# Optimization experiments

Measured on AMD Instinct MI355X. Metric: run time of the kernel, lower is better.

Reference implementation:

```python
import jax, jax.numpy as jnp
import numpy as np
from jax import lax

EPS = 1e-6


def _layernorm(x, g, b, eps=1e-5):
    m = x.mean(-1, keepdims=True)
    v = x.var(-1, keepdims=True)
    return (x - m) / jnp.sqrt(v + eps) * g + b


def _causal_conv(x, w, b, dilation):
    # x: [B,S,D], w: [K, D_in, D_out] -> causal (left) padded dilated conv + GELU, residual
    k = w.shape[0]
    pad = (k - 1) * dilation
    y = lax.conv_general_dilated(
        x, w, window_strides=(1,), padding=[(pad, 0)], rhs_dilation=(dilation,),
        dimension_numbers=('NWC', 'WIO', 'NWC'))
    return x + jax.nn.gelu(y + b)


def setup_inputs() -> dict:
    key = jax.random.key(0)
    B, S, D, DC, N_LTM, K_WM, KS = 4, 2048, 1024, 256, 768, 8, 5
    ks = jax.random.split(key, 24)
    sc = 0.02

    def n(k, shape, scale=sc):
        return jax.random.normal(k, shape, jnp.float32) * scale

    return {
        'x': jax.random.normal(ks[0], (B, S, D), jnp.float32),
        'cache': jax.random.normal(ks[1], (B, N_LTM, DC), jnp.float32),
        'wm': jax.random.normal(ks[2], (B, K_WM, DC + 1), jnp.float32),
        # LTM read projections
        'Wq_ltm': n(ks[3], (D, DC)), 'Wo_ltm': n(ks[4], (DC, D)), 'wg_ltm': n(ks[5], (D,)),
        # WM read projections
        'Wq_wm': n(ks[6], (D, DC)), 'Wo_wm': n(ks[7], (DC, D)), 'wg_wm': n(ks[8], (D,)),
        # causal dilated conv stack (2 layers, k=5, dilations 1 and 2)
        'conv1_w': n(ks[9], (KS, D, D)), 'conv1_b': jnp.zeros((D,), jnp.float32),
        'conv2_w': n(ks[10], (KS, D, D)), 'conv2_b': jnp.zeros((D,), jnp.float32),
        'ln_g': jnp.ones((D,), jnp.float32), 'ln_b': jnp.zeros((D,), jnp.float32),
        # WM write (learned slot keys for addressing)
        'Wqw_wm': n(ks[11], (D, DC)), 'Ww_wm': n(ks[12], (D, DC)),
        'wm_keys': n(ks[13], (K_WM, DC), 1.0), 'wgw_wm': n(ks[14], (D,)),
        # LTM write (content-based addressing against cache)
        'Wqw_ltm': n(ks[15], (D, DC)), 'Ww_ltm': n(ks[16], (D, DC)), 'wgw_ltm': n(ks[17], (D,)),
    }


def reference(x, cache, wm, Wq_ltm, Wo_ltm, wg_ltm, Wq_wm, Wo_wm, wg_wm,
              conv1_w, conv1_b, conv2_w, conv2_b, ln_g, ln_b,
              Wqw_wm, Ww_wm, wm_keys, wgw_wm, Wqw_ltm, Ww_ltm, wgw_ltm):
    DC = cache.shape[-1]
    inv_sqrt = 1.0 / jnp.sqrt(jnp.float32(DC))

    # ---- LTM READ: content-addressed soft read, gated residual blend ----
    q = x @ Wq_ltm                                                  # [B,S,DC]
    attn = jax.nn.softmax(jnp.einsum('bsd,bnd->bsn', q, cache) * inv_sqrt, -1)
    read = jnp.einsum('bsn,bnd->bsd', attn, cache)                  # [B,S,DC]
    gate = jax.nn.sigmoid(x @ wg_ltm)[..., None]                    # [B,S,1]
    x_ltm = x + gate * (read @ Wo_ltm)

    # ---- WM READ (read_decay=0.0 -> wm unchanged by read) ----
    content = wm[..., :DC]                                          # [B,Kw,DC]
    q2 = x_ltm @ Wq_wm
    attn2 = jax.nn.softmax(jnp.einsum('bsd,bkd->bsk', q2, content) * inv_sqrt, -1)
    read2 = jnp.einsum('bsk,bkd->bsd', attn2, content)
    gate2 = jax.nn.sigmoid(x_ltm @ wg_wm)[..., None]
    x_enh = x_ltm + gate2 * (read2 @ Wo_wm)

    # ---- COMPUTE: causal dilated conv stack + post-LayerNorm ----
    h = _causal_conv(x_enh, conv1_w, conv1_b, 1)
    h = _causal_conv(h, conv2_w, conv2_b, 2)
    out = _layernorm(h, ln_g, ln_b)                                 # [B,S,D]

    # ---- WM WRITE: gated soft-WTA addressing vs learned slot keys ----
    qw = out @ Wqw_wm                                               # [B,S,DC]
    aw = jax.nn.softmax(jnp.einsum('bsd,kd->bsk', qw, wm_keys) * inv_sqrt, -1)
    gw = jax.nn.sigmoid(out @ wgw_wm)[..., None]                    # [B,S,1]
    w = gw * aw                                                     # [B,S,Kw]
    tot = w.sum(1)                                                  # [B,Kw]
    c = out @ Ww_wm                                                 # [B,S,DC]
    avg = jnp.einsum('bsk,bsd->bkd', w, c) / (tot[..., None] + EPS)
    alpha = jnp.clip(tot, 0.0, 1.0)[..., None]
    new_content = (1.0 - alpha) * content + alpha * avg
    new_valid = jnp.clip(wm[..., DC] + tot, 0.0, 1.0)               # validity channel
    updated_wm = jnp.concatenate([new_content, new_valid[..., None]], -1)

    # ---- LTM WRITE: gated soft blended write, content-addressed vs cache ----
    ql = out @ Wqw_ltm
    al = jax.nn.softmax(jnp.einsum('bsd,bnd->bsn', ql, cache) * inv_sqrt, -1)
    gl = jax.nn.sigmoid(out @ wgw_ltm)[..., None]
    wl = gl * al                                                    # [B,S,N]
    totl = wl.sum(1)                                                # [B,N]
    cl = out @ Ww_ltm
    avgl = jnp.einsum('bsn,bsd->bnd', wl, cl) / (totl[..., None] + EPS)
    alphal = jnp.clip(totl, 0.0, 1.0)[..., None]
    updated_cache = (1.0 - alphal) * cache + alphal * avgl

    return (out, updated_cache, updated_wm)
```

## Files before the change

kernel.cpp:

```cpp
#include <hip/hip_runtime.h>
#include <stdint.h>

typedef unsigned short u16;
typedef unsigned int u32;
typedef __attribute__((ext_vector_type(8))) short s16x8;
typedef __attribute__((ext_vector_type(4))) float f32x4;

__device__ __forceinline__ float bf2f(u16 u) {
    return __builtin_bit_cast(float, (u32)u << 16);
}
__device__ __forceinline__ u16 f2bf(float f) {
    u32 u = __builtin_bit_cast(u32, f);
    u += 0x7FFFu + ((u >> 16) & 1u);
    return (u16)(u >> 16);
}
__device__ __forceinline__ void unpk4(uint2 r, float* o) {
    o[0] = bf2f((u16)(r.x & 0xffff)); o[1] = bf2f((u16)(r.x >> 16));
    o[2] = bf2f((u16)(r.y & 0xffff)); o[3] = bf2f((u16)(r.y >> 16));
}

__device__ __forceinline__ void gl16(const u16* g, u16* l) {
    __builtin_amdgcn_global_load_lds(
        (const __attribute__((address_space(1))) u32*)(const void*)g,
        (__attribute__((address_space(3))) u32*)(void*)l, 16, 0, 0);
}

#define BAR() { __builtin_amdgcn_sched_barrier(0); __builtin_amdgcn_s_barrier(); __builtin_amdgcn_sched_barrier(0); }

template<int DIL>
__global__ __launch_bounds__(512) void conv8_k(
    const u16* __restrict__ Apad, const u16* __restrict__ Bw,
    u16* __restrict__ Cb0, u16* __restrict__ Cb1)
{
    __shared__ u16 sA[2][16384];
    __shared__ u16 sB[2][16384];
    const int tid  = threadIdx.x;
    const int wid  = tid >> 6;
    const int lane = tid & 63;
    const int wr = (wid >> 2) * 128;
    const int wc = (wid & 3) * 64;
    const int lr = lane & 15;
    const int kq = lane >> 4;
    const int sw = (blockIdx.x & 7) * 32 + (blockIdx.x >> 3);
    const int z    = sw >> 7;
    const int bn0  = ((sw >> 5) & 3) * 256;
    const int xm   = sw & 31;
    const int batch = xm >> 3;
    const int m0b   = (xm & 7) * 256;
    const int kbeg  = z * 2560;
    const u16* Ab = Apad + (long)batch * 2056 * 1024;

    const int row0 = tid >> 3;
    const int g0   = (tid & 7) ^ (row0 & 7);

    f32x4 acc[8][4] = {};
    s16x8 aF[4][2], bF[4][2];

    auto stageA = [&](int nb, int kt, int h) {
        const int ktabs = kbeg + kt * 64;
        const int tap = ktabs >> 10;
        const long rbase = (long)(8 + m0b + h * 128 + (tap - 4) * DIL) * 1024
                           + (ktabs & 1023) + g0 * 8;
        u16* dst = &sA[nb][h * 8192 + tid * 8];
        gl16(Ab + rbase + (long)row0 * 1024, dst);
        gl16(Ab + rbase + (long)(row0 + 64) * 1024, dst + 4096);
    };
    auto stageB = [&](int nb, int kt, int h) {
        const int ktabs = kbeg + kt * 64;
        const long rbase = (long)(bn0 + h * 128) * 5120 + ktabs + g0 * 8;
        u16* dst = &sB[nb][h * 8192 + tid * 8];
        gl16(Bw + rbase + (long)row0 * 5120, dst);
        gl16(Bw + rbase + (long)(row0 + 64) * 5120, dst + 4096);
    };
    auto readA = [&](int nb, int mq) {
        #pragma unroll
        for (int m = 0; m < 4; m++) {
            const int row = wr + (mq * 4 + m) * 16 + lr;
            #pragma unroll
            for (int ks = 0; ks < 2; ks++) {
                const int chunk = ks * 4 + kq;
                aF[m][ks] = *(const s16x8*)&sA[nb][row * 64 + ((chunk ^ (row & 7)) << 3)];
            }
        }
    };
    auto readB4 = [&](int nb, int nq) {
        #pragma unroll
        for (int n = 0; n < 2; n++) {
            const int row = wc + (nq * 2 + n) * 16 + lr;
            #pragma unroll
            for (int ks = 0; ks < 2; ks++) {
                const int chunk = ks * 4 + kq;
                bF[nq * 2 + n][ks] = *(const s16x8*)&sB[nb][row * 64 + ((chunk ^ (row & 7)) << 3)];
            }
        }
    };

#define MFQ(MQ, NQ) \
    { __builtin_amdgcn_s_setprio(1); \
      _Pragma("unroll") \
      for (int m = 0; m < 4; m++) { \
        _Pragma("unroll") \
        for (int n = 0; n < 2; n++) { \
          _Pragma("unroll") \
          for (int ks = 0; ks < 2; ks++) \
            acc[(MQ)*4+m][(NQ)*2+n] = __builtin_amdgcn_mfma_f32_16x16x32_bf16( \
                aF[m][ks], bF[(NQ)*2+n][ks], acc[(MQ)*4+m][(NQ)*2+n], 0, 0, 0); \
        } } \
      __builtin_amdgcn_s_setprio(0); }

    stageB(0, 0, 0); stageB(0, 0, 1); stageA(0, 0, 0); stageA(0, 0, 1);

    const int NT = 40;
    for (int t = 0; t < NT; ++t) {
        const int nb = t & 1;
        asm volatile("s_waitcnt vmcnt(4)" ::: "memory");
        BAR();
        readB4(nb, 0); readB4(nb, 1);
        if (t + 1 < NT) { stageB(nb ^ 1, t + 1, 0); stageB(nb ^ 1, t + 1, 1); }
        if (t + 1 < NT) { asm volatile("s_waitcnt vmcnt(4)" ::: "memory"); }
        else            { asm volatile("s_waitcnt vmcnt(0)" ::: "memory"); }
        BAR();
        readA(nb, 0);
        MFQ(0, 0); MFQ(0, 1);
        if (t + 1 < NT) { stageA(nb ^ 1, t + 1, 0); stageA(nb ^ 1, t + 1, 1); }
        readA(nb, 1);
        MFQ(1, 0); MFQ(1, 1);
    }
#undef MFQ

    u16* C = (z ? Cb1 : Cb0) + (long)batch * 2048 * 1024;
    #pragma unroll
    for (int m = 0; m < 8; m++) {
        #pragma unroll
        for (int n = 0; n < 4; n++) {
            const int cc = bn0 + wc + n * 16 + lr;
            #pragma unroll
            for (int j = 0; j < 4; j++) {
                const int r = m0b + wr + m * 16 + kq * 4 + j;
                C[(long)r * 1024 + cc] = f2bf(acc[m][n][j]);
            }
        }
    }
}

template<int AL, int BL, int EPI, int TN, int KS, int SWZ>
__global__ __launch_bounds__(256) void gemm_bf16(
    const u16* __restrict__ A, const u16* __restrict__ B,
    float* __restrict__ Cf, u16* __restrict__ Cb,
    const float* __restrict__ res, const float* __restrict__ gate,
    int M, int N, int K, int lda, int ldb,
    long aBS, long bBS, long cBS,
    u16* __restrict__ Pp, long pStride, int nby)
{
    constexpr int NFRAG = TN / 32;
    __shared__ u16 sA[128 * 32];
    __shared__ u16 sB[TN * 32];
    const int tid  = threadIdx.x;
    const int lane = tid & 63;
    const int wave = tid >> 6;
    const int wr = (wave >> 1) * 64;
    const int wc = (wave & 1) * (TN / 2);

    int bidx, bidy;
    if (SWZ) {
        const int nb  = gridDim.x;
        const int cpx = nb >> 3;
        const int bf  = blockIdx.x;
        const int sw  = (bf & 7) * cpx + (bf >> 3);
        bidx = sw / nby; bidy = sw - bidx * nby;
    } else {
        bidx = blockIdx.x; bidy = blockIdx.y;
    }
    const int m0 = bidx * 128;
    const int n0 = bidy * TN;
    const int zz = blockIdx.z;
    const long bz = (KS > 1) ? (zz / KS) : zz;
    const int ks  = (KS > 1) ? (zz % KS) : 0;
    const u16* Ab = A + bz * aBS;
    const u16* Bb = B + bz * bBS;

    f32x4 acc[4][NFRAG] = {};
    const int lr = lane & 15;
    const int lk = (lane >> 4) << 3;
    const int ar0 = tid >> 2;
    const int akg = (tid & 3) << 3;

    const int Kp = K / KS;
    const int kbeg = ks * Kp, kend = kbeg + Kp;

    for (int kk = kbeg; kk < kend; kk += 32) {
        __syncthreads();
        if (AL == 0) {
            gl16(Ab + (long)(m0 + ar0) * lda + kk + akg,      sA + tid * 8);
            gl16(Ab + (long)(m0 + ar0 + 64) * lda + kk + akg, sA + tid * 8 + 2048);
        } else {
            for (int t = tid; t < 512; t += 256) {
                int row = t & 127, kg = (t >> 7) << 3;
                u32 w0[4];
                #pragma unroll
                for (int j2 = 0; j2 < 4; j2++) {
                    u16 lo = Ab[(long)(kk + kg + 2*j2    ) * lda + m0 + row];
                    u16 hi = Ab[(long)(kk + kg + 2*j2 + 1) * lda + m0 + row];
                    w0[j2] = (u32)lo | ((u32)hi << 16);
                }
                uint4 v; v.x = w0[0]; v.y = w0[1]; v.z = w0[2]; v.w = w0[3];
                *reinterpret_cast<uint4*>(sA + row * 32 + kg) = v;
            }
        }
        if (BL == 1) {
            gl16(Bb + (long)(n0 + ar0) * ldb + kk + akg, sB + tid * 8);
            if (TN == 128)
                gl16(Bb + (long)(n0 + ar0 + 64) * ldb + kk + akg, sB + tid * 8 + 2048);
        } else {
            for (int t = tid; t < TN * 4; t += 256) {
                int col = t & (TN - 1), kg = (t / TN) << 3;
                u32 w0[4];
                #pragma unroll
                for (int j2 = 0; j2 < 4; j2++) {
                    u16 lo = Bb[(long)(kk + kg + 2*j2    ) * ldb + n0 + col];
                    u16 hi = Bb[(long)(kk + kg + 2*j2 + 1) * ldb + n0 + col];
                    w0[j2] = (u32)lo | ((u32)hi << 16);
                }
                uint4 v; v.x = w0[0]; v.y = w0[1]; v.z = w0[2]; v.w = w0[3];
                *reinterpret_cast<uint4*>(sB + col * 32 + kg) = v;
            }
        }
        __syncthreads();
        s16x8 aF[4], bF[NFRAG];
        #pragma unroll
        for (int m = 0; m < 4; m++)
            aF[m] = *reinterpret_cast<const s16x8*>(sA + (wr + m*16 + lr) * 32 + lk);
        #pragma unroll
        for (int n = 0; n < NFRAG; n++)
            bF[n] = *reinterpret_cast<const s16x8*>(sB + (wc + n*16 + lr) * 32 + lk);
        #pragma unroll
        for (int m = 0; m < 4; m++)
            #pragma unroll
            for (int n = 0; n < NFRAG; n++)
                acc[m][n] = __builtin_amdgcn_mfma_f32_16x16x32_bf16(aF[m], bF[n], acc[m][n], 0, 0, 0);
    }

    const int rj = (lane >> 4) << 2;
    if (KS > 1) {
        u16* Pb = Pp + (long)ks * pStride + bz * cBS;
        #pragma unroll
        for (int m = 0; m < 4; m++)
            #pragma unroll
            for (int n = 0; n < NFRAG; n++) {
                const int cc = n0 + wc + n*16 + lr;
                #pragma unroll
                for (int j = 0; j < 4; j++) {
                    const int r = m0 + wr + m*16 + rj + j;
                    Pb[(long)r * N + cc] = f2bf(acc[m][n][j]);
                }
            }
        return;
    }

    float* Cfb = Cf + bz * cBS;
    #pragma unroll
    for (int m = 0; m < 4; m++) {
        #pragma unroll
        for (int n = 0; n < NFRAG; n++) {
            const int cc = n0 + wc + n*16 + lr;
            #pragma unroll
            for (int j = 0; j < 4; j++) {
                const int r = m0 + wr + m*16 + rj + j;
                const long idx = (long)r * N + cc;
                const float v = acc[m][n][j];
                if (EPI == 0) {
                    Cb[bz * cBS + idx] = f2bf(v);
                } else if (EPI == 1) {
                    Cfb[idx] = v;
                } else {
                    float o = res[idx] + gate[r] * v;
                    Cfb[idx] = o;
                    if (EPI == 2) Cb[idx] = f2bf(o);
                }
            }
        }
    }
}

template<int KS, int BF>
__global__ __launch_bounds__(256) void ksum_k(
    const u16* __restrict__ Pp, long pStride,
    float* __restrict__ outf, u16* __restrict__ outb, int n4)
{
    int i = blockIdx.x * 256 + threadIdx.x;
    if (i >= n4) return;
    float s[4] = {0.f, 0.f, 0.f, 0.f};
    #pragma unroll
    for (int k = 0; k < KS; k++) {
        uint2 r = reinterpret_cast<const uint2*>(Pp + (long)k * pStride)[i];
        float v[4]; unpk4(r, v);
        s[0] += v[0]; s[1] += v[1]; s[2] += v[2]; s[3] += v[3];
    }
    if (BF) {
        u32 lo = (u32)f2bf(s[0]) | ((u32)f2bf(s[1]) << 16);
        u32 hi = (u32)f2bf(s[2]) | ((u32)f2bf(s[3]) << 16);
        reinterpret_cast<uint2*>(outb)[i] = make_uint2(lo, hi);
    } else {
        float4 o; o.x = s[0]; o.y = s[1]; o.z = s[2]; o.w = s[3];
        reinterpret_cast<float4*>(outf)[i] = o;
    }
}

__global__ void zero_init_k(u16* __restrict__ a, u16* __restrict__ b,
                            float* __restrict__ tot, float* __restrict__ totl)
{
    int i = blockIdx.x * 256 + threadIdx.x;
    int bt = i >> 12, j = i & 4095;
    long off = (long)bt * (2056L * 1024 / 2) + j;
    reinterpret_cast<u32*>(a)[off] = 0u;
    reinterpret_cast<u32*>(b)[off] = 0u;
    if (i < 32) tot[i] = 0.f;
    if (i < 3072) totl[i] = 0.f;
}

__global__ void f32_to_bf16_k(const float* __restrict__ in, u16* __restrict__ out, int n4)
{
    int i = blockIdx.x * 256 + threadIdx.x;
    if (i < n4) {
        float4 v = reinterpret_cast<const float4*>(in)[i];
        u32 lo = (u32)f2bf(v.x) | ((u32)f2bf(v.y) << 16);
        u32 hi = (u32)f2bf(v.z) | ((u32)f2bf(v.w) << 16);
        reinterpret_cast<uint2*>(out)[i] = make_uint2(lo, hi);
    }
}

__global__ __launch_bounds__(256) void tr_all_k(
    const float* __restrict__ Wq_ltm, const float* __restrict__ Wq_wm,
    const float* __restrict__ Wqw_wm, const float* __restrict__ Ww_wm,
    const float* __restrict__ Wqw_ltm, const float* __restrict__ Ww_ltm,
    const float* __restrict__ Wo_ltm, const float* __restrict__ conv1_w,
    const float* __restrict__ conv2_w, const float* __restrict__ cache,
    u16* __restrict__ WqLt, u16* __restrict__ WqWt, u16* __restrict__ WbigT,
    u16* __restrict__ WoLt, u16* __restrict__ c1wt, u16* __restrict__ c2wt,
    u16* __restrict__ cache_t)
{
    int b = blockIdx.x;
    const float* in; u16* out; int R, C, l;
    if (b < 1536) {
        l = b & 255; R = 1024; C = 256;
        int m = b >> 8;
        if      (m == 0) { in = Wq_ltm;  out = WqLt; }
        else if (m == 1) { in = Wq_wm;   out = WqWt; }
        else if (m == 2) { in = Wqw_wm;  out = WbigT; }
        else if (m == 3) { in = Ww_wm;   out = WbigT + 262144; }
        else if (m == 4) { in = Wqw_ltm; out = WbigT + 524288; }
        else             { in = Ww_ltm;  out = WbigT + 786432; }
    } else if (b < 1792) {
        l = b - 1536; in = Wo_ltm; out = WoLt; R = 256; C = 1024;
    } else if (b < 6912) {
        l = b - 1792; in = conv1_w; out = c1wt; R = 5120; C = 1024;
    } else if (b < 12032) {
        l = b - 6912; in = conv2_w; out = c2wt; R = 5120; C = 1024;
    } else {
        int lb = b - 12032;
        int z = lb / 192; l = lb % 192;
        in = cache + (long)z * 196608; out = cache_t + (long)z * 196608;
        R = 768; C = 256;
    }
    const int ct = C >> 5;
    const int c0 = (l % ct) * 32, r0 = (l / ct) * 32;
    __shared__ float tile[32][33];
    int tx = threadIdx.x & 31, ty = threadIdx.x >> 5;
    #pragma unroll
    for (int i = 0; i < 32; i += 8)
        tile[ty + i][tx] = in[(long)(r0 + ty + i) * C + c0 + tx];
    __syncthreads();
    #pragma unroll
    for (int i = 0; i < 32; i += 8)
        out[(long)(c0 + ty + i) * R + r0 + tx] = f2bf(tile[tx][ty + i]);
}

__global__ __launch_bounds__(256) void cw_k(
    const float* __restrict__ wm, const float* __restrict__ Wo, float* __restrict__ CW)
{
    int blk = blockIdx.x;
    const float* wrow = wm + (long)(blk >> 3) * 2056 + (blk & 7) * 257;
    int c = threadIdx.x;
    float a0 = 0.f, a1 = 0.f, a2 = 0.f, a3 = 0.f;
    for (int dd = 0; dd < 256; dd++) {
        float w = wrow[dd];
        const float* wo = Wo + (long)dd * 1024;
        a0 += w * wo[c]; a1 += w * wo[c + 256];
        a2 += w * wo[c + 512]; a3 += w * wo[c + 768];
    }
    float* o = CW + (long)blk * 1024;
    o[c] = a0; o[c + 256] = a1; o[c + 512] = a2; o[c + 768] = a3;
}

__global__ __launch_bounds__(256) void wc_k(
    const float* __restrict__ wm, const u16* __restrict__ WqWt, float* __restrict__ WC)
{
    int blk = blockIdx.x;
    const float* wrow = wm + (long)(blk >> 3) * 2056 + (blk & 7) * 257;
    int c = threadIdx.x;
    float a0 = 0.f, a1 = 0.f, a2 = 0.f, a3 = 0.f;
    for (int j = 0; j < 256; j++) {
        float w = wrow[j];
        const u16* wq = WqWt + (long)j * 1024;
        a0 += bf2f(wq[c])       * w;
        a1 += bf2f(wq[c + 256]) * w;
        a2 += bf2f(wq[c + 512]) * w;
        a3 += bf2f(wq[c + 768]) * w;
    }
    float* o = WC + (long)blk * 1024;
    o[c] = a0; o[c + 256] = a1; o[c + 512] = a2; o[c + 768] = a3;
}

__global__ __launch_bounds__(256) void gemv_sigmoid_k(
    const float* __restrict__ X, const float* __restrict__ w,
    float* __restrict__ out)
{
    int row  = blockIdx.x * 4 + (threadIdx.x >> 6);
    int lane = threadIdx.x & 63;
    const float* xr = X + (long)row * 1024;
    float s = 0.f;
    for (int i = lane; i < 1024; i += 64) s += xr[i] * w[i];
    #pragma unroll
    for (int o = 32; o > 0; o >>= 1) s += __shfl_down(s, o);
    if (lane == 0) out[row] = 1.f / (1.f + __expf(-s));
}

__global__ __launch_bounds__(256) void softmax768_k(
    const float* __restrict__ scores, u16* __restrict__ out,
    const float* __restrict__ gate)
{
    __shared__ float s4[4], s4b[4];
    int row = blockIdx.x;
    int t = threadIdx.x;
    const float* sr = scores + (long)row * 768;
    float v[3];
    float m = -1e30f;
    #pragma unroll
    for (int i = 0; i < 3; i++) { v[i] = sr[t + i*256] * 0.0625f; m = fmaxf(m, v[i]); }
    float wm_ = m;
    #pragma unroll
    for (int o = 32; o > 0; o >>= 1) wm_ = fmaxf(wm_, __shfl_down(wm_, o));
    if ((t & 63) == 0) s4[t >> 6] = wm_;
    __syncthreads();
    float bm = fmaxf(fmaxf(s4[0], s4[1]), fmaxf(s4[2], s4[3]));
    float sum = 0.f;
    #pragma unroll
    for (int i = 0; i < 3; i++) { v[i] = __expf(v[i] - bm); sum += v[i]; }
    #pragma unroll
    for (int o = 32; o > 0; o >>= 1) sum += __shfl_down(sum, o);
    if ((t & 63) == 0) s4b[t >> 6] = sum;
    __syncthreads();
    float bs = s4b[0] + s4b[1] + s4b[2] + s4b[3];
    float g = gate ? gate[row] : 1.0f;
    float inv = g / bs;
    u16* orow = out + (long)row * 768;
    #pragma unroll
    for (int i = 0; i < 3; i++) orow[t + i*256] = f2bf(v[i] * inv);
}

__global__ __launch_bounds__(256) void wm_read_fused_k(
    const float* __restrict__ WC, const float* __restrict__ CW,
    const float* __restrict__ wg, const float* __restrict__ res,
    float* __restrict__ outf, u16* __restrict__ outb)
{
    __shared__ float sred[8][4];
    __shared__ float sg4[4];
    __shared__ float sa[8];
    __shared__ float gsh;
    int row = blockIdx.x;
    int b = row >> 11;
    int d = threadIdx.x, lane = d & 63, wave = d >> 6;
    long orow = (long)row * 1024;
    float rv0 = res[orow + d];
    float rv1 = res[orow + d + 256];
    float rv2 = res[orow + d + 512];
    float rv3 = res[orow + d + 768];
    float gp = rv0 * wg[d] + rv1 * wg[d + 256] + rv2 * wg[d + 512] + rv3 * wg[d + 768];
    #pragma unroll
    for (int o = 32; o > 0; o >>= 1) gp += __shfl_down(gp, o);
    if (lane == 0) sg4[wave] = gp;
    const float* wcb = WC + (long)b * 8192;
    #pragma unroll
    for (int k = 0; k < 8; k++) {
        const float* w = wcb + k * 1024;
        float v = rv0 * w[d] + rv1 * w[d + 256] + rv2 * w[d + 512] + rv3 * w[d + 768];
        #pragma unroll
        for (int o = 32; o > 0; o >>= 1) v += __shfl_down(v, o);
        if (lane == 0) sred[k][wave] = v;
    }
    __syncthreads();
    if (d < 8) sa[d] = (sred[d][0] + sred[d][1] + sred[d][2] + sred[d][3]) * 0.0625f;
    if (d == 0) gsh = 1.f / (1.f + __expf(-(sg4[0] + sg4[1] + sg4[2] + sg4[3])));
    __syncthreads();
    float m = sa[0];
    #pragma unroll
    for (int k = 1; k < 8; k++) m = fmaxf(m, sa[k]);
    float e[8], sum = 0.f;
    #pragma unroll
    for (int k = 0; k < 8; k++) { e[k] = __expf(sa[k] - m); sum += e[k]; }
    float inv = 1.f / sum;
    #pragma unroll
    for (int k = 0; k < 8; k++) e[k] *= inv;
    float g = gsh;
    const float* cwb = CW + (long)b * 8192;
    long prow = ((long)(row >> 11) * 2056 + 8 + (row & 2047)) * 1024;
    float rv[4] = { rv0, rv1, rv2, rv3 };
    #pragma unroll
    for (int j = 0; j < 4; j++) {
        int c = d + j * 256;
        float acc = 0.f;
        #pragma unroll
        for (int k = 0; k < 8; k++) acc += e[k] * cwb[k * 1024 + c];
        float o = rv[j] + g * acc;
        outf[orow + c] = o;
        outb[prow + c] = f2bf(o);
    }
}

template<int PAD>
__global__ __launch_bounds__(256) void gelu_reduce_k(
    const u16* __restrict__ p0, const u16* __restrict__ p1, const float4* __restrict__ res,
    const float* __restrict__ bias, float4* __restrict__ outf, u16* __restrict__ outb)
{
    int i4 = blockIdx.x * 256 + threadIdx.x;
    int r = i4 >> 8, c4 = (i4 & 255) << 2;
    float a[4], b[4];
    unpk4(reinterpret_cast<const uint2*>(p0)[i4], a);
    unpk4(reinterpret_cast<const uint2*>(p1)[i4], b);
    float4 rr = res[i4];
    float4 bi = *reinterpret_cast<const float4*>(bias + c4);
    float o[4];
    float y0 = a[0] + b[0] + bi.x, y1 = a[1] + b[1] + bi.y;
    float y2 = a[2] + b[2] + bi.z, y3 = a[3] + b[3] + bi.w;
    const float C0 = 0.79788456080286535588f, C1 = 0.044715f;
    o[0] = rr.x + 0.5f * y0 * (1.f + tanhf(C0 * (y0 + C1 * y0 * y0 * y0)));
    o[1] = rr.y + 0.5f * y1 * (1.f + tanhf(C0 * (y1 + C1 * y1 * y1 * y1)));
    o[2] = rr.z + 0.5f * y2 * (1.f + tanhf(C0 * (y2 + C1 * y2 * y2 * y2)));
    o[3] = rr.w + 0.5f * y3 * (1.f + tanhf(C0 * (y3 + C1 * y3 * y3 * y3)));
    float4 ov; ov.x = o[0]; ov.y = o[1]; ov.z = o[2]; ov.w = o[3];
    outf[i4] = ov;
    if (PAD) {
        long prow = ((long)(r >> 11) * 2056 + 8 + (r & 2047)) * 1024 + c4;
        u32 lo = (u32)f2bf(o[0]) | ((u32)f2bf(o[1]) << 16);
        u32 hi = (u32)f2bf(o[2]) | ((u32)f2bf(o[3]) << 16);
        *reinterpret_cast<uint2*>(outb + prow) = make_uint2(lo, hi);
    }
}

__global__ __launch_bounds__(256) void gelu_ln_k(
    const u16* __restrict__ p0, const u16* __restrict__ p1,
    const float4* __restrict__ res, const float* __restrict__ bias,
    const float* __restrict__ g, const float* __restrict__ b,
    float* __restrict__ outf, u16* __restrict__ outb)
{
    __shared__ float rs[4], rss[4];
    int row = blockIdx.x, t = threadIdx.x;
    long i4 = (long)row * 256 + t;
    float a[4], pb[4];
    unpk4(reinterpret_cast<const uint2*>(p0)[i4], a);
    unpk4(reinterpret_cast<const uint2*>(p1)[i4], pb);
    float4 rr = res[i4];
    float4 bi = reinterpret_cast<const float4*>(bias)[t];
    const float C0 = 0.79788456080286535588f, C1 = 0.044715f;
    float y0 = a[0] + pb[0] + bi.x, y1 = a[1] + pb[1] + bi.y;
    float y2 = a[2] + pb[2] + bi.z, y3 = a[3] + pb[3] + bi.w;
    float o0 = rr.x + 0.5f * y0 * (1.f + tanhf(C0 * (y0 + C1 * y0 * y0 * y0)));
    float o1 = rr.y + 0.5f * y1 * (1.f + tanhf(C0 * (y1 + C1 * y1 * y1 * y1)));
    float o2 = rr.z + 0.5f * y2 * (1.f + tanhf(C0 * (y2 + C1 * y2 * y2 * y2)));
    float o3 = rr.w + 0.5f * y3 * (1.f + tanhf(C0 * (y3 + C1 * y3 * y3 * y3)));
    float s  = o0 + o1 + o2 + o3;
    float ss = o0*o0 + o1*o1 + o2*o2 + o3*o3;
    #pragma unroll
    for (int o = 32; o > 0; o >>= 1) { s += __shfl_down(s, o); ss += __shfl_down(ss, o); }
    if ((t & 63) == 0) { rs[t >> 6] = s; rss[t >> 6] = ss; }
    __syncthreads();
    float S = rs[0]+rs[1]+rs[2]+rs[3];
    float SS = rss[0]+rss[1]+rss[2]+rss[3];
    float mean = S * (1.f/1024.f);
    float var  = SS * (1.f/1024.f) - mean*mean;
    float rstd = rsqrtf(var + 1e-5f);
    float4 gg = reinterpret_cast<const float4*>(g)[t];
    float4 bv = reinterpret_cast<const float4*>(b)[t];
    float4 y;
    y.x = (o0-mean)*rstd*gg.x + bv.x;
    y.y = (o1-mean)*rstd*gg.y + bv.y;
    y.z = (o2-mean)*rstd*gg.z + bv.z;
    y.w = (o3-mean)*rstd*gg.w + bv.w;
    reinterpret_cast<float4*>(outf)[i4] = y;
    u32 lo = (u32)f2bf(y.x) | ((u32)f2bf(y.y) << 16);
    u32 hi = (u32)f2bf(y.z) | ((u32)f2bf(y.w) << 16);
    reinterpret_cast<uint2*>(outb)[i4] = make_uint2(lo, hi);
}

__global__ __launch_bounds__(256) void attn8_wg_k(
    const u16* __restrict__ q, const float* __restrict__ xo,
    const float* __restrict__ w1, const float* __restrict__ w2,
    const u16* __restrict__ keys, float* __restrict__ wD,
    float* __restrict__ gateb2)
{
    __shared__ float sred[8][4];
    __shared__ float sa[8];
    __shared__ float sg1[4], sg2[4];
    __shared__ float g1sh;
    int row = blockIdx.x;
    int d = threadIdx.x, lane = d & 63, wave = d >> 6;
    float qv = bf2f(q[(long)row * 1024 + d]);
    float4 xr  = reinterpret_cast<const float4*>(xo + (long)row * 1024)[d];
    float4 w1v = reinterpret_cast<const float4*>(w1)[d];
    float4 w2v = reinterpret_cast<const float4*>(w2)[d];
    float s1 = xr.x*w1v.x + xr.y*w1v.y + xr.z*w1v.z + xr.w*w1v.w;
    float s2 = xr.x*w2v.x + xr.y*w2v.y + xr.z*w2v.z + xr.w*w2v.w;
    #pragma unroll
    for (int o = 32; o > 0; o >>= 1) { s1 += __shfl_down(s1, o); s2 += __shfl_down(s2, o); }
    if (lane == 0) { sg1[wave] = s1; sg2[wave] = s2; }
    #pragma unroll
    for (int k = 0; k < 8; k++) {
        float v = qv * bf2f(keys[k * 256 + d]);
        #pragma unroll
        for (int o = 32; o > 0; o >>= 1) v += __shfl_down(v, o);
        if (lane == 0) sred[k][wave] = v;
    }
    __syncthreads();
    if (d < 8) sa[d] = (sred[d][0] + sred[d][1] + sred[d][2] + sred[d][3]) * 0.0625f;
    if (d == 0) {
        g1sh = 1.f / (1.f + __expf(-(sg1[0] + sg1[1] + sg1[2] + sg1[3])));
        gateb2[row] = 1.f / (1.f + __expf(-(sg2[0] + sg2[1] + sg2[2] + sg2[3])));
    }
    __syncthreads();
    if (d < 8) {
        float m = sa[0];
        #pragma unroll
        for (int k = 1; k < 8; k++) m = fmaxf(m, sa[k]);
        float e = __expf(sa[d] - m), sum = 0.f;
        #pragma unroll
        for (int k = 0; k < 8; k++) sum += __expf(sa[k] - m);
        wD[(long)row * 8 + d] = g1sh * e / sum;
    }
}

__global__ __launch_bounds__(256) void tot8_k(const float* __restrict__ wD, float* __restrict__ tot)
{
    __shared__ float s4[4];
    int b = blockIdx.y;
    int s = blockIdx.x * 256 + threadIdx.x;
    const float* p = wD + ((long)b * 2048 + s) * 8;
    float v[8];
    #pragma unroll
    for (int k = 0; k < 8; k++) v[k] = p[k];
    for (int k = 0; k < 8; k++) {
        float xv = v[k];
        #pragma unroll
        for (int o = 32; o > 0; o >>= 1) xv += __shfl_down(xv, o);
        if ((threadIdx.x & 63) == 0) s4[threadIdx.x >> 6] = xv;
        __syncthreads();
        if (threadIdx.x == 0) atomicAdd(&tot[b*8 + k], s4[0]+s4[1]+s4[2]+s4[3]);
        __syncthreads();
    }
}

__global__ __launch_bounds__(256) void wm_avg_partial_k(
    const float* __restrict__ wD, const u16* __restrict__ cw, float* __restrict__ part)
{
    int blk = blockIdx.x;
    int b = blk >> 6, k = (blk >> 3) & 7, ch = blk & 7;
    int d = threadIdx.x;
    const float* wp = wD + ((long)b * 2048 + ch * 256) * 8 + k;
    const u16*   cp = cw + ((long)b * 2048 + ch * 256) * 1024 + 256 + d;
    float acc = 0.f;
    for (int s = 0; s < 256; s++) acc += wp[s * 8] * bf2f(cp[(long)s * 1024]);
    part[(long)blk * 256 + d] = acc;
}

__global__ __launch_bounds__(256) void wm_final_k(
    const float* __restrict__ part, const float* __restrict__ wm,
    const float* __restrict__ tot, float* __restrict__ out)
{
    int bk = blockIdx.x;
    int d = threadIdx.x;
    float acc = 0.f;
    #pragma unroll
    for (int ch = 0; ch < 8; ch++) acc += part[((long)bk * 8 + ch) * 256 + d];
    float t = tot[bk];
    float alpha = fminf(fmaxf(t, 0.f), 1.f);
    float avg = acc / (t + 1e-6f);
    long base = (long)(bk >> 3) * 2056 + (bk & 7) * 257;
    out[base + d] = (1.f - alpha) * wm[base + d] + alpha * avg;
    if (d == 0) out[base + 256] = fminf(fmaxf(wm[base + 256] + t, 0.f), 1.f);
}

__global__ void colsum_wl_k(const u16* __restrict__ wl, float* __restrict__ totl)
{
    int b = blockIdx.z;
    int n = blockIdx.x * 256 + threadIdx.x;
    int s0 = blockIdx.y * 256;
    const u16* p = wl + ((long)b * 2048 + s0) * 768 + n;
    float acc = 0.f;
    for (int s = 0; s < 256; s++) acc += bf2f(p[(long)s * 768]);
    atomicAdd(&totl[b * 768 + n], acc);
}

__global__ void cache_blend_k(const float* __restrict__ cache, const float* __restrict__ Sg,
                              const float* __restrict__ totl, float* __restrict__ out)
{
    long i = (long)blockIdx.x * 256 + threadIdx.x;
    int bn = (int)(i >> 8);
    float t = totl[bn];
    float a = fminf(fmaxf(t, 0.f), 1.f);
    out[i] = (1.f - a) * cache[i] + a * (Sg[i] / (t + 1e-6f));
}

extern "C" void kernel_launch(void* const* d_in, const int* in_sizes, int n_in,
                              void* d_out, int out_size, void* d_ws, size_t ws_size,
                              hipStream_t stream)
{
    const int D = 1024, DC = 256, NL = 768;
    const long MS = 8192;
    const long SB = 2048;

    const float* x       = (const float*)d_in[0];
    const float* cache   = (const float*)d_in[1];
    const float* wm      = (const float*)d_in[2];
    const float* Wq_ltm  = (const float*)d_in[3];
    const float* Wo_ltm  = (const float*)d_in[4];
    const float* wg_ltm  = (const float*)d_in[5];
    const float* Wq_wm   = (const float*)d_in[6];
    const float* Wo_wm   = (const float*)d_in[7];
    const float* wg_wm   = (const float*)d_in[8];
    const float* conv1_w = (const float*)d_in[9];
    const float* conv1_b = (const float*)d_in[10];
    const float* conv2_w = (const float*)d_in[11];
    const float* conv2_b = (const float*)d_in[12];
    const float* ln_g    = (const float*)d_in[13];
    const float* ln_b    = (const float*)d_in[14];
    const float* Wqw_wm  = (const float*)d_in[15];
    const float* Ww_wm   = (const float*)d_in[16];
    const float* wm_keys = (const float*)d_in[17];
    const float* wgw_wm  = (const float*)d_in[18];
    const float* Wqw_ltm = (const float*)d_in[19];
    const float* Ww_ltm  = (const float*)d_in[20];
    const float* wgw_ltm = (const float*)d_in[21];

    float* out_f     = (float*)d_out;
    float* cache_out = out_f + 8388608;
    float* wm_out    = out_f + 8388608 + 786432;

    char* ws = (char*)d_ws;
    size_t off = 0;
    auto alloc = [&](size_t bytes) -> char* {
        char* p = ws + off;
        off = (off + bytes + 255) & ~(size_t)255;
        return p;
    };
    u16* WqLt    = (u16*)alloc((size_t)D*DC*2);
    u16* WoLt    = (u16*)alloc((size_t)D*DC*2);
    u16* WqWt    = (u16*)alloc((size_t)D*DC*2);
    u16* WbigT   = (u16*)alloc((size_t)D*D*2);
    u16* c1wt    = (u16*)alloc((size_t)5*D*D*2);
    u16* c2wt    = (u16*)alloc((size_t)5*D*D*2);
    u16* cache_b = (u16*)alloc((size_t)4*NL*DC*2);
    u16* cache_t = (u16*)alloc((size_t)4*NL*DC*2);
    u16* keys_b  = (u16*)alloc((size_t)8*DC*2);
    u16* act0    = (u16*)alloc((size_t)MS*D*2);
    u16* act1    = (u16*)alloc((size_t)MS*D*2);
    u16* xpad1   = (u16*)alloc((size_t)4*2056*1024*2);
    u16* xpad2   = (u16*)alloc((size_t)4*2056*1024*2);
    u16* qb      = (u16*)alloc((size_t)MS*DC*2);
    u16* attnb   = (u16*)alloc((size_t)MS*NL*2);
    u16* readb   = (u16*)alloc((size_t)MS*DC*2);
    float* fact0 = (float*)alloc((size_t)MS*D*4);
    float* fact1 = (float*)alloc((size_t)MS*D*4);
    u16* Pu      = (u16*)alloc((size_t)16777216*2);
    float* CW    = (float*)alloc((size_t)4*8*D*4);
    float* WC    = (float*)alloc((size_t)4*8*D*4);
    float* gateb = (float*)alloc((size_t)MS*4);
    float* gateb2= (float*)alloc((size_t)MS*4);
    float* wD    = (float*)alloc((size_t)MS*8*4);
    float* tot   = (float*)alloc((size_t)4*8*4);
    float* totl  = (float*)alloc((size_t)4*NL*4);
    float* part  = (float*)alloc((size_t)256*256*4);
    float* avglS = (float*)alloc((size_t)4*NL*DC*4);
    float* scores = fact0;
    u16*   qbig   = act0;

    auto cv = [&](const float* in, u16* out, long n) {
        long n4 = n / 4;
        f32_to_bf16_k<<<dim3((unsigned)((n4 + 255) / 256)), 256, 0, stream>>>(in, out, (int)n4);
    };

    zero_init_k<<<64, 256, 0, stream>>>(xpad1, xpad2, tot, totl);
    cv(x, act0, MS * D);
    cv(cache, cache_b, (long)4 * NL * DC);
    cv(wm_keys, keys_b, 8 * DC);
    tr_all_k<<<12800, 256, 0, stream>>>(
        Wq_ltm, Wq_wm, Wqw_wm, Ww_wm, Wqw_ltm, Ww_ltm, Wo_ltm, conv1_w, conv2_w, cache,
        WqLt, WqWt, WbigT, WoLt, c1wt, c2wt, cache_t);
    cw_k<<<32, 256, 0, stream>>>(wm, Wo_wm, CW);
    wc_k<<<32, 256, 0, stream>>>(wm, WqWt, WC);

    gemm_bf16<0,1,0,64,4,1><<<dim3(256,1,4), 256, 0, stream>>>(
        act0, WqLt, nullptr, nullptr, nullptr, nullptr,
        8192,256,1024,1024,1024, 0,0,0, Pu, 2097152L, 4);
    ksum_k<4,1><<<2048, 256, 0, stream>>>(Pu, 2097152L, nullptr, qb, 524288);
    gemv_sigmoid_k<<<2048, 256, 0, stream>>>(x, wg_ltm, gateb);
    gemm_bf16<0,1,1,128,1,1><<<dim3(96,1,4), 256, 0, stream>>>(
        qb, cache_b, scores, nullptr, nullptr, nullptr,
        2048,768,256,256,256, SB*256, (long)NL*DC, SB*768, nullptr, 0, 6);
    softmax768_k<<<8192, 256, 0, stream>>>(scores, attnb, nullptr);
    gemm_bf16<0,1,0,64,2,1><<<dim3(64,1,8), 256, 0, stream>>>(
        attnb, cache_t, nullptr, nullptr, nullptr, nullptr,
        2048,256,768,768,768, SB*768, (long)NL*DC, SB*256, Pu, 2097152L, 4);
    ksum_k<2,1><<<2048, 256, 0, stream>>>(Pu, 2097152L, nullptr, readb, 524288);
    gemm_bf16<0,1,5,128,1,1><<<dim3(512,1,1), 256, 0, stream>>>(
        readb, WoLt, fact0, nullptr, x, gateb,
        8192,1024,256,256,256, 0,0,0, nullptr, 0, 8);

    wm_read_fused_k<<<8192, 256, 0, stream>>>(WC, CW, wg_wm, fact0, fact1, xpad1);

    conv8_k<1><<<256, 512, 0, stream>>>(xpad1, c1wt, Pu, Pu + 8388608);
    gelu_reduce_k<1><<<8192, 256, 0, stream>>>(
        Pu, Pu + 8388608, (const float4*)fact1, conv1_b, (float4*)fact0, xpad2);
    conv8_k<2><<<256, 512, 0, stream>>>(xpad2, c2wt, Pu, Pu + 8388608);
    gelu_ln_k<<<8192, 256, 0, stream>>>(
        Pu, Pu + 8388608, (const float4*)fact0, conv2_b, ln_g, ln_b, out_f, act1);

    gemm_bf16<0,1,0,128,1,1><<<dim3(512,1,1), 256, 0, stream>>>(
        act1, WbigT, nullptr, qbig, nullptr, nullptr,
        8192,1024,1024,1024,1024, 0,0,0, nullptr, 0, 8);
    attn8_wg_k<<<8192, 256, 0, stream>>>(qbig, out_f, wgw_wm, wgw_ltm, keys_b, wD, gateb2);
    tot8_k<<<dim3(8, 4), 256, 0, stream>>>(wD, tot);
    wm_avg_partial_k<<<256, 256, 0, stream>>>(wD, qbig, part);
    wm_final_k<<<32, 256, 0, stream>>>(part, wm, tot, wm_out);

    gemm_bf16<0,1,1,128,1,1><<<dim3(96,1,4), 256, 0, stream>>>(
        qbig + 512, cache_b, scores, nullptr, nullptr, nullptr,
        2048,768,256,1024,256, SB*1024, (long)NL*DC, SB*768, nullptr, 0, 6);
    softmax768_k<<<8192, 256, 0, stream>>>(scores, attnb, gateb2);
    colsum_wl_k<<<dim3(3, 8, 4), 256, 0, stream>>>(attnb, totl);
    gemm_bf16<1,0,1,64,4,0><<<dim3(6,4,16), 256, 0, stream>>>(
        attnb, qbig + 768, nullptr, nullptr, nullptr, nullptr,
        768,256,2048,768,1024, SB*768, SB*1024, 196608L, Pu, 786432L, 0);
    ksum_k<4,0><<<768, 256, 0, stream>>>(Pu, 786432L, avglS, nullptr, 196608);
    cache_blend_k<<<3072, 256, 0, stream>>>(cache, avglS, totl, cache_out);

    (void)in_sizes; (void)n_in; (void)out_size; (void)ws_size;
}
```

Before: 531.0 us.

## Merge prep kernels into one launch, store scores as bf16, simplify conv grid

Combines zero-init, the fp32-to-bf16 conversions, the weight transposes and the CW/WC precomputes into a single prep kernel to cut launch count, with WC now read from fp32 Wq_wm rather than the transposed bf16 copy. Attention scores are written as bf16 instead of fp32 before softmax, halving that traffic at some precision cost. The conv kernel's swizzled 1D block mapping is replaced by a plain 3D grid, which may change L2 locality.

```diff
diff --git a/kernel.cpp b/kernel.cpp
--- a/kernel.cpp
+++ b/kernel.cpp
@@ -41,13 +41,10 @@
     const int wc = (wid & 3) * 64;
     const int lr = lane & 15;
     const int kq = lane >> 4;
-    const int sw = (blockIdx.x & 7) * 32 + (blockIdx.x >> 3);
-    const int z    = sw >> 7;
-    const int bn0  = ((sw >> 5) & 3) * 256;
-    const int xm   = sw & 31;
-    const int batch = xm >> 3;
-    const int m0b   = (xm & 7) * 256;
-    const int kbeg  = z * 2560;
+    const int batch = blockIdx.x >> 3;
+    const int m0b   = (blockIdx.x & 7) * 256;
+    const int bn0   = blockIdx.y * 256;
+    const int kbeg  = blockIdx.z * 2560;
     const u16* Ab = Apad + (long)batch * 2056 * 1024;
 
     const int row0 = tid >> 3;
@@ -128,7 +125,7 @@
     }
 #undef MFQ
 
-    u16* C = (z ? Cb1 : Cb0) + (long)batch * 2048 * 1024;
+    u16* C = (blockIdx.z ? Cb1 : Cb0) + (long)batch * 2048 * 1024;
     #pragma unroll
     for (int m = 0; m < 8; m++) {
         #pragma unroll
@@ -306,109 +303,113 @@
     }
 }
 
-__global__ void zero_init_k(u16* __restrict__ a, u16* __restrict__ b,
-                            float* __restrict__ tot, float* __restrict__ totl)
-{
-    int i = blockIdx.x * 256 + threadIdx.x;
-    int bt = i >> 12, j = i & 4095;
-    long off = (long)bt * (2056L * 1024 / 2) + j;
-    reinterpret_cast<u32*>(a)[off] = 0u;
-    reinterpret_cast<u32*>(b)[off] = 0u;
-    if (i < 32) tot[i] = 0.f;
-    if (i < 3072) totl[i] = 0.f;
-}
-
-__global__ void f32_to_bf16_k(const float* __restrict__ in, u16* __restrict__ out, int n4)
-{
-    int i = blockIdx.x * 256 + threadIdx.x;
-    if (i < n4) {
+__global__ __launch_bounds__(256) void prep_k(
+    const float* __restrict__ x, const float* __restrict__ cache,
+    const float* __restrict__ wm_keys, const float* __restrict__ wm,
+    const float* __restrict__ Wo_wm, const float* __restrict__ Wq_wm,
+    const float* __restrict__ Wq_ltm, const float* __restrict__ Wqw_wm,
+    const float* __restrict__ Ww_wm, const float* __restrict__ Wqw_ltm,
+    const float* __restrict__ Ww_ltm, const float* __restrict__ Wo_ltm,
+    const float* __restrict__ conv1_w, const float* __restrict__ conv2_w,
+    u16* __restrict__ xpad1, u16* __restrict__ xpad2,
+    float* __restrict__ tot, float* __restrict__ totl,
+    u16* __restrict__ act0, u16* __restrict__ cache_b, u16* __restrict__ keys_b,
+    u16* __restrict__ WqLt, u16* __restrict__ WqWt, u16* __restrict__ WbigT,
+    u16* __restrict__ WoLt, u16* __restrict__ c1wt, u16* __restrict__ c2wt,
+    u16* __restrict__ cache_t, float* __restrict__ CW, float* __restrict__ WC)
+{
+    __shared__ float tile[32][33];
+    int b = blockIdx.x;
+    int tid = threadIdx.x;
+
+    if (b < 64) {
+        int i = b * 256 + tid;
+        int bt = i >> 12, j = i & 4095;
+        long offp = (long)bt * (2056L * 1024 / 2) + j;
+        reinterpret_cast<u32*>(xpad1)[offp] = 0u;
+        reinterpret_cast<u32*>(xpad2)[offp] = 0u;
+        if (i < 32) tot[i] = 0.f;
+        if (i < 3072) totl[i] = 0.f;
+        return;
+    }
+    b -= 64;
+    if (b < 8192 + 768 + 2) {
+        const float* in; u16* out; int i;
+        if (b < 8192)      { in = x;       out = act0;    i = b * 256 + tid; }
+        else if (b < 8960) { in = cache;   out = cache_b; i = (b - 8192) * 256 + tid; }
+        else               { in = wm_keys; out = keys_b;  i = (b - 8960) * 256 + tid; }
         float4 v = reinterpret_cast<const float4*>(in)[i];
         u32 lo = (u32)f2bf(v.x) | ((u32)f2bf(v.y) << 16);
         u32 hi = (u32)f2bf(v.z) | ((u32)f2bf(v.w) << 16);
         reinterpret_cast<uint2*>(out)[i] = make_uint2(lo, hi);
-    }
-}
-
-__global__ __launch_bounds__(256) void tr_all_k(
-    const float* __restrict__ Wq_ltm, const float* __restrict__ Wq_wm,
-    const float* __restrict__ Wqw_wm, const float* __restrict__ Ww_wm,
-    const float* __restrict__ Wqw_ltm, const float* __restrict__ Ww_ltm,
-    const float* __restrict__ Wo_ltm, const float* __restrict__ conv1_w,
-    const float* __restrict__ conv2_w, const float* __restrict__ cache,
-    u16* __restrict__ WqLt, u16* __restrict__ WqWt, u16* __restrict__ WbigT,
-    u16* __restrict__ WoLt, u16* __restrict__ c1wt, u16* __restrict__ c2wt,
-    u16* __restrict__ cache_t)
-{
-    int b = blockIdx.x;
-    const float* in; u16* out; int R, C, l;
-    if (b < 1536) {
-        l = b & 255; R = 1024; C = 256;
-        int m = b >> 8;
-        if      (m == 0) { in = Wq_ltm;  out = WqLt; }
-        else if (m == 1) { in = Wq_wm;   out = WqWt; }
-        else if (m == 2) { in = Wqw_wm;  out = WbigT; }
-        else if (m == 3) { in = Ww_wm;   out = WbigT + 262144; }
-        else if (m == 4) { in = Wqw_ltm; out = WbigT + 524288; }
-        else             { in = Ww_ltm;  out = WbigT + 786432; }
-    } else if (b < 1792) {
-        l = b - 1536; in = Wo_ltm; out = WoLt; R = 256; C = 1024;
-    } else if (b < 6912) {
-        l = b - 1792; in = conv1_w; out = c1wt; R = 5120; C = 1024;
-    } else if (b < 12032) {
-        l = b - 6912; in = conv2_w; out = c2wt; R = 5120; C = 1024;
-    } else {
-        int lb = b - 12032;
-        int z = lb / 192; l = lb % 192;
-        in = cache + (long)z * 196608; out = cache_t + (long)z * 196608;
-        R = 768; C = 256;
-    }
-    const int ct = C >> 5;
-    const int c0 = (l % ct) * 32, r0 = (l / ct) * 32;
-    __shared__ float tile[32][33];
-    int tx = threadIdx.x & 31, ty = threadIdx.x >> 5;
-    #pragma unroll
-    for (int i = 0; i < 32; i += 8)
-        tile[ty + i][tx] = in[(long)(r0 + ty + i) * C + c0 + tx];
-    __syncthreads();
-    #pragma unroll
-    for (int i = 0; i < 32; i += 8)
-        out[(long)(c0 + ty + i) * R + r0 + tx] = f2bf(tile[tx][ty + i]);
-}
-
-__global__ __launch_bounds__(256) void cw_k(
-    const float* __restrict__ wm, const float* __restrict__ Wo, float* __restrict__ CW)
-{
-    int blk = blockIdx.x;
-    const float* wrow = wm + (long)(blk >> 3) * 2056 + (blk & 7) * 257;
-    int c = threadIdx.x;
-    float a0 = 0.f, a1 = 0.f, a2 = 0.f, a3 = 0.f;
-    for (int dd = 0; dd < 256; dd++) {
-        float w = wrow[dd];
-        const float* wo = Wo + (long)dd * 1024;
-        a0 += w * wo[c]; a1 += w * wo[c + 256];
-        a2 += w * wo[c + 512]; a3 += w * wo[c + 768];
-    }
-    float* o = CW + (long)blk * 1024;
-    o[c] = a0; o[c + 256] = a1; o[c + 512] = a2; o[c + 768] = a3;
-}
-
-__global__ __launch_bounds__(256) void wc_k(
-    const float* __restrict__ wm, const u16* __restrict__ WqWt, float* __restrict__ WC)
-{
-    int blk = blockIdx.x;
-    const float* wrow = wm + (long)(blk >> 3) * 2056 + (blk & 7) * 257;
-    int c = threadIdx.x;
-    float a0 = 0.f, a1 = 0.f, a2 = 0.f, a3 = 0.f;
-    for (int j = 0; j < 256; j++) {
-        float w = wrow[j];
-        const u16* wq = WqWt + (long)j * 1024;
-        a0 += bf2f(wq[c])       * w;
-        a1 += bf2f(wq[c + 256]) * w;
-        a2 += bf2f(wq[c + 512]) * w;
-        a3 += bf2f(wq[c + 768]) * w;
-    }
-    float* o = WC + (long)blk * 1024;
-    o[c] = a0; o[c + 256] = a1; o[c + 512] = a2; o[c + 768] = a3;
+        return;
+    }
+    b -= 8962;
+    if (b < 12800) {
+        const float* in; u16* out; int R, C, l;
+        if (b < 1536) {
+            l = b & 255; R = 1024; C = 256;
+            int m = b >> 8;
+            if      (m == 0) { in = Wq_ltm;  out = WqLt; }
+            else if (m == 1) { in = Wq_wm;   out = WqWt; }
+            else if (m == 2) { in = Wqw_wm;  out = WbigT; }
+            else if (m == 3) { in = Ww_wm;   out = WbigT + 262144; }
+            else if (m == 4) { in = Wqw_ltm; out = WbigT + 524288; }
+            else             { in = Ww_ltm;  out = WbigT + 786432; }
+        } else if (b < 1792) {
+            l = b - 1536; in = Wo_ltm; out = WoLt; R = 256; C = 1024;
+        } else if (b < 6912) {
+            l = b - 1792; in = conv1_w; out = c1wt; R = 5120; C = 1024;
+        } else if (b < 12032) {
+            l = b - 6912; in = conv2_w; out = c2wt; R = 5120; C = 1024;
+        } else {
+            int lb = b - 12032;
+            int z = lb / 192; l = lb % 192;
+            in = cache + (long)z * 196608; out = cache_t + (long)z * 196608;
+            R = 768; C = 256;
+        }
+        const int ct = C >> 5;
+        const int c0 = (l % ct) * 32, r0 = (l / ct) * 32;
+        int tx = tid & 31, ty = tid >> 5;
+        #pragma unroll
+        for (int i = 0; i < 32; i += 8)
+            tile[ty + i][tx] = in[(long)(r0 + ty + i) * C + c0 + tx];
+        __syncthreads();
+        #pragma unroll
+        for (int i = 0; i < 32; i += 8)
+            out[(long)(c0 + ty + i) * R + r0 + tx] = f2bf(tile[tx][ty + i]);
+        return;
+    }
+    b -= 12800;
+    if (b < 32) {
+        const float* wrow = wm + (long)(b >> 3) * 2056 + (b & 7) * 257;
+        int c = tid;
+        float a0 = 0.f, a1 = 0.f, a2 = 0.f, a3 = 0.f;
+        for (int dd = 0; dd < 256; dd++) {
+            float w = wrow[dd];
+            const float* wo = Wo_wm + (long)dd * 1024;
+            a0 += w * wo[c]; a1 += w * wo[c + 256];
+            a2 += w * wo[c + 512]; a3 += w * wo[c + 768];
+        }
+        float* o = CW + (long)b * 1024;
+        o[c] = a0; o[c + 256] = a1; o[c + 512] = a2; o[c + 768] = a3;
+        return;
+    }
+    b -= 32;
+    {
+        const float* wrow = wm + (long)(b >> 3) * 2056 + (b & 7) * 257;
+        int c = tid;
+        float a0 = 0.f, a1 = 0.f, a2 = 0.f, a3 = 0.f;
+        for (int j = 0; j < 256; j++) {
+            float w = wrow[j];
+            a0 += Wq_wm[(long)(c      ) * 256 + j] * w;
+            a1 += Wq_wm[(long)(c + 256) * 256 + j] * w;
+            a2 += Wq_wm[(long)(c + 512) * 256 + j] * w;
+            a3 += Wq_wm[(long)(c + 768) * 256 + j] * w;
+        }
+        float* o = WC + (long)b * 1024;
+        o[c] = a0; o[c + 256] = a1; o[c + 512] = a2; o[c + 768] = a3;
+    }
 }
 
 __global__ __launch_bounds__(256) void gemv_sigmoid_k(
@@ -426,17 +427,17 @@
 }
 
 __global__ __launch_bounds__(256) void softmax768_k(
-    const float* __restrict__ scores, u16* __restrict__ out,
+    const u16* __restrict__ scores, u16* __restrict__ out,
     const float* __restrict__ gate)
 {
     __shared__ float s4[4], s4b[4];
     int row = blockIdx.x;
     int t = threadIdx.x;
-    const float* sr = scores + (long)row * 768;
+    const u16* sr = scores + (long)row * 768;
     float v[3];
     float m = -1e30f;
     #pragma unroll
-    for (int i = 0; i < 3; i++) { v[i] = sr[t + i*256] * 0.0625f; m = fmaxf(m, v[i]); }
+    for (int i = 0; i < 3; i++) { v[i] = bf2f(sr[t + i*256]) * 0.0625f; m = fmaxf(m, v[i]); }
     float wm_ = m;
     #pragma unroll
     for (int o = 32; o > 0; o >>= 1) wm_ = fmaxf(wm_, __shfl_down(wm_, o));
@@ -779,33 +780,23 @@
     float* totl  = (float*)alloc((size_t)4*NL*4);
     float* part  = (float*)alloc((size_t)256*256*4);
     float* avglS = (float*)alloc((size_t)4*NL*DC*4);
-    float* scores = fact0;
     u16*   qbig   = act0;
 
-    auto cv = [&](const float* in, u16* out, long n) {
-        long n4 = n / 4;
-        f32_to_bf16_k<<<dim3((unsigned)((n4 + 255) / 256)), 256, 0, stream>>>(in, out, (int)n4);
-    };
-
-    zero_init_k<<<64, 256, 0, stream>>>(xpad1, xpad2, tot, totl);
-    cv(x, act0, MS * D);
-    cv(cache, cache_b, (long)4 * NL * DC);
-    cv(wm_keys, keys_b, 8 * DC);
-    tr_all_k<<<12800, 256, 0, stream>>>(
-        Wq_ltm, Wq_wm, Wqw_wm, Ww_wm, Wqw_ltm, Ww_ltm, Wo_ltm, conv1_w, conv2_w, cache,
-        WqLt, WqWt, WbigT, WoLt, c1wt, c2wt, cache_t);
-    cw_k<<<32, 256, 0, stream>>>(wm, Wo_wm, CW);
-    wc_k<<<32, 256, 0, stream>>>(wm, WqWt, WC);
+    prep_k<<<21890, 256, 0, stream>>>(
+        x, cache, wm_keys, wm, Wo_wm, Wq_wm,
+        Wq_ltm, Wqw_wm, Ww_wm, Wqw_ltm, Ww_ltm, Wo_ltm, conv1_w, conv2_w,
+        xpad1, xpad2, tot, totl, act0, cache_b, keys_b,
+        WqLt, WqWt, WbigT, WoLt, c1wt, c2wt, cache_t, CW, WC);
 
     gemm_bf16<0,1,0,64,4,1><<<dim3(256,1,4), 256, 0, stream>>>(
         act0, WqLt, nullptr, nullptr, nullptr, nullptr,
         8192,256,1024,1024,1024, 0,0,0, Pu, 2097152L, 4);
     ksum_k<4,1><<<2048, 256, 0, stream>>>(Pu, 2097152L, nullptr, qb, 524288);
     gemv_sigmoid_k<<<2048, 256, 0, stream>>>(x, wg_ltm, gateb);
-    gemm_bf16<0,1,1,128,1,1><<<dim3(96,1,4), 256, 0, stream>>>(
-        qb, cache_b, scores, nullptr, nullptr, nullptr,
+    gemm_bf16<0,1,0,128,1,1><<<dim3(96,1,4), 256, 0, stream>>>(
+        qb, cache_b, nullptr, Pu, nullptr, nullptr,
         2048,768,256,256,256, SB*256, (long)NL*DC, SB*768, nullptr, 0, 6);
-    softmax768_k<<<8192, 256, 0, stream>>>(scores, attnb, nullptr);
+    softmax768_k<<<8192, 256, 0, stream>>>(Pu, attnb, nullptr);
     gemm_bf16<0,1,0,64,2,1><<<dim3(64,1,8), 256, 0, stream>>>(
         attnb, cache_t, nullptr, nullptr, nullptr, nullptr,
         2048,256,768,768,768, SB*768, (long)NL*DC, SB*256, Pu, 2097152L, 4);
@@ -816,10 +807,10 @@
 
     wm_read_fused_k<<<8192, 256, 0, stream>>>(WC, CW, wg_wm, fact0, fact1, xpad1);
 
-    conv8_k<1><<<256, 512, 0, stream>>>(xpad1, c1wt, Pu, Pu + 8388608);
+    conv8_k<1><<<dim3(32,4,2), 512, 0, stream>>>(xpad1, c1wt, Pu, Pu + 8388608);
     gelu_reduce_k<1><<<8192, 256, 0, stream>>>(
         Pu, Pu + 8388608, (const float4*)fact1, conv1_b, (float4*)fact0, xpad2);
-    conv8_k<2><<<256, 512, 0, stream>>>(xpad2, c2wt, Pu, Pu + 8388608);
+    conv8_k<2><<<dim3(32,4,2), 512, 0, stream>>>(xpad2, c2wt, Pu, Pu + 8388608);
     gelu_ln_k<<<8192, 256, 0, stream>>>(
         Pu, Pu + 8388608, (const float4*)fact0, conv2_b, ln_g, ln_b, out_f, act1);
 
@@ -831,10 +822,10 @@
     wm_avg_partial_k<<<256, 256, 0, stream>>>(wD, qbig, part);
     wm_final_k<<<32, 256, 0, stream>>>(part, wm, tot, wm_out);
 
-    gemm_bf16<0,1,1,128,1,1><<<dim3(96,1,4), 256, 0, stream>>>(
-        qbig + 512, cache_b, scores, nullptr, nullptr, nullptr,
+    gemm_bf16<0,1,0,128,1,1><<<dim3(96,1,4), 256, 0, stream>>>(
+        qbig + 512, cache_b, nullptr, Pu, nullptr, nullptr,
         2048,768,256,1024,256, SB*1024, (long)NL*DC, SB*768, nullptr, 0, 6);
-    softmax768_k<<<8192, 256, 0, stream>>>(scores, attnb, gateb2);
+    softmax768_k<<<8192, 256, 0, stream>>>(Pu, attnb, gateb2);
     colsum_wl_k<<<dim3(3, 8, 4), 256, 0, stream>>>(attnb, totl);
     gemm_bf16<1,0,1,64,4,0><<<dim3(6,4,16), 256, 0, stream>>>(
         attnb, qbig + 768, nullptr, nullptr, nullptr, nullptr,
```

New measurement: 502.8 us. -5.3%, faster.
